# Kernel tuning notes

Measured on AMD Instinct MI355X. Metric: run time of the kernel, lower is better.

Reference implementation:

```python
import jax, jax.numpy as jnp
import numpy as np

NEG_SLOPE = 0.1
K = 3  # kernel_size

def lrelu(x):
    return jnp.where(x >= 0, x, NEG_SLOPE * x)

def setup_inputs() -> dict:
    key = jax.random.key(0)
    ks = jax.random.split(key, 10)
    B, C, H, W = 16, 64, 128, 128
    DEG, RED = 512, 8
    s = 0.02
    return {
        "feat": jax.random.normal(ks[0], (B, C, H, W), jnp.float32),
        "deg": jax.random.normal(ks[1], (B, DEG, 8, 8), jnp.float32),
        # adaptive_size: Linear(deg_fsize -> C), no bias; torch weight [out,in]
        "W_size": jax.random.normal(ks[2], (C, DEG), jnp.float32) * s,
        # kernel net: Linear(C -> C//red), Linear(C//red -> C*K*K)
        "W_k1": jax.random.normal(ks[3], (C // RED, C), jnp.float32) * s,
        "W_k2": jax.random.normal(ks[4], (C * K * K, C // RED), jnp.float32) * s,
        # 1x1 conv C_in -> C_out with bias (stored as [out,in])
        "W_conv": jax.random.normal(ks[5], (C, C), jnp.float32) * s,
        "b_conv": jax.random.normal(ks[6], (C,), jnp.float32) * s,
        # CA layer: 1x1 conv deg_fsize -> C, then C -> C//red -> C
        "W_ac": jax.random.normal(ks[7], (C, DEG), jnp.float32) * s,
        "W_du1": jax.random.normal(ks[8], (C // RED, C), jnp.float32) * s,
        "W_du2": jax.random.normal(ks[9], (C, C // RED), jnp.float32) * s,
    }

def reference(feat, deg, W_size, W_k1, W_k2, W_conv, b_conv, W_ac, W_du1, W_du2):
    b, c, h, w = feat.shape
    # degradation pooled to a vector: AdaptiveAvgPool2d((1,1)) == mean over HW
    dvec = deg.mean(axis=(2, 3))                      # [B, deg_fsize]
    f = dvec @ W_size.T                               # [B, C]
    # per-sample dynamic depthwise kernels
    kern = lrelu(f @ W_k1.T) @ W_k2.T                 # [B, C*K*K]
    kern = kern.reshape(b * c, 1, K, K)               # [B*C, 1, K, K]
    out = jax.lax.conv_general_dilated(
        feat.reshape(1, b * c, h, w), kern,
        window_strides=(1, 1), padding=[((K - 1) // 2,) * 2] * 2,
        feature_group_count=b * c,
        dimension_numbers=("NCHW", "OIHW", "NCHW"))
    out = lrelu(out).reshape(b, c, h, w)
    # trailing 1x1 conv with bias
    out = jnp.einsum("bchw,oc->bohw", out, W_conv) + b_conv[None, :, None, None]
    # CA branch
    fa = dvec @ W_ac.T                                # [B, C]
    att = jax.nn.sigmoid(lrelu(fa @ W_du1.T) @ W_du2.T)  # [B, C_out]
    return out + feat * att[:, :, None, None]
```

## Files before the change

kernel.cpp:

```cpp
#include <hip/hip_runtime.h>
#include <math.h>

#define NEG_SLOPE 0.1f

typedef __attribute__((ext_vector_type(8))) short short8;
typedef __attribute__((ext_vector_type(4))) short short4v;
typedef __attribute__((ext_vector_type(4))) float floatx4;

__device__ __forceinline__ float lrelu(float x) { return x >= 0.0f ? x : NEG_SLOPE * x; }

__device__ __forceinline__ unsigned short f2bf(float x) {
  unsigned u = __float_as_uint(x);
  return (unsigned short)((u + 0x7fffu + ((u >> 16) & 1u)) >> 16);
}

__device__ __forceinline__ float wave_sum64(float v) {
  #pragma unroll
  for (int s = 32; s > 0; s >>= 1) v += __shfl_xor(v, s, 64);
  return v;
}

__global__ __launch_bounds__(256) void prep_kernel(
    const float* __restrict__ deg, const float* __restrict__ W_size,
    const float* __restrict__ W_k1, const float* __restrict__ W_k2,
    const float* __restrict__ W_ac, const float* __restrict__ W_du1,
    const float* __restrict__ W_du2, float* __restrict__ kern_ws,
    float* __restrict__ att_ws) {
  const int b = blockIdx.x;
  const int t = threadIdx.x;
  __shared__ float dvec[512];
  __shared__ float fbuf[64], fabuf[64];
  __shared__ float t1s[8], t2s[8];

  const float* degb = deg + (size_t)b * 32768;
  const int half = t & 1, row0 = t >> 1;
  #pragma unroll
  for (int u = 0; u < 4; ++u) {
    const int d = row0 + u * 128;
    const float* p = degb + (size_t)d * 64 + half * 32;
    float4 x0 = *(const float4*)(p);
    float4 x1 = *(const float4*)(p + 4);
    float4 x2 = *(const float4*)(p + 8);
    float4 x3 = *(const float4*)(p + 12);
    float4 x4 = *(const float4*)(p + 16);
    float4 x5 = *(const float4*)(p + 20);
    float4 x6 = *(const float4*)(p + 24);
    float4 x7 = *(const float4*)(p + 28);
    float s = (x0.x + x0.y + x0.z + x0.w) + (x1.x + x1.y + x1.z + x1.w) +
              (x2.x + x2.y + x2.z + x2.w) + (x3.x + x3.y + x3.z + x3.w) +
              (x4.x + x4.y + x4.z + x4.w) + (x5.x + x5.y + x5.z + x5.w) +
              (x6.x + x6.y + x6.z + x6.w) + (x7.x + x7.y + x7.z + x7.w);
    s += __shfl_xor(s, 1, 64);
    if (half == 0) dvec[d] = s * (1.0f / 64.0f);
  }
  __syncthreads();

  {
    const int c = t >> 2, q = t & 3;
    const float* w1 = W_size + (size_t)c * 512;
    const float* w2 = W_ac + (size_t)c * 512;
    float p1 = 0.0f, p2 = 0.0f;
    #pragma unroll 4
    for (int kk = 0; kk < 32; ++kk) {
      const int e = kk * 16 + q * 4;
      float4 d4 = *(const float4*)&dvec[e];
      float4 a4 = *(const float4*)(w1 + e);
      float4 b4 = *(const float4*)(w2 + e);
      p1 += d4.x * a4.x + d4.y * a4.y + d4.z * a4.z + d4.w * a4.w;
      p2 += d4.x * b4.x + d4.y * b4.y + d4.z * b4.z + d4.w * b4.w;
    }
    p1 += __shfl_xor(p1, 1, 64); p1 += __shfl_xor(p1, 2, 64);
    p2 += __shfl_xor(p2, 1, 64); p2 += __shfl_xor(p2, 2, 64);
    if (q == 0) { fbuf[c] = p1; fabuf[c] = p2; }
  }
  __syncthreads();

  const int wave = t >> 6, lane = t & 63;
  if (wave == 0) {
    float v = fbuf[lane];
    #pragma unroll
    for (int rr = 0; rr < 8; ++rr) {
      float p = wave_sum64(v * W_k1[rr * 64 + lane]);
      if (lane == 0) t1s[rr] = lrelu(p);
    }
  } else if (wave == 1) {
    float v = fabuf[lane];
    #pragma unroll
    for (int rr = 0; rr < 8; ++rr) {
      float p = wave_sum64(v * W_du1[rr * 64 + lane]);
      if (lane == 0) t2s[rr] = lrelu(p);
    }
  }
  __syncthreads();

  for (int i = t; i < 576; i += 256) {
    float4 wa0 = *(const float4*)&W_k2[i * 8];
    float4 wa1 = *(const float4*)&W_k2[i * 8 + 4];
    kern_ws[b * 576 + i] =
        t1s[0] * wa0.x + t1s[1] * wa0.y + t1s[2] * wa0.z + t1s[3] * wa0.w +
        t1s[4] * wa1.x + t1s[5] * wa1.y + t1s[6] * wa1.z + t1s[7] * wa1.w;
  }
  if (t < 64) {
    float4 wa0 = *(const float4*)&W_du2[t * 8];
    float4 wa1 = *(const float4*)&W_du2[t * 8 + 4];
    float s = t2s[0] * wa0.x + t2s[1] * wa0.y + t2s[2] * wa0.z + t2s[3] * wa0.w +
              t2s[4] * wa1.x + t2s[5] * wa1.y + t2s[6] * wa1.z + t2s[7] * wa1.w;
    att_ws[b * 64 + t] = 1.0f / (1.0f + expf(-s));
  }
}

__global__ __launch_bounds__(256, 5) void fused_kernel(
    const float* __restrict__ feat, const float* __restrict__ W_conv,
    const float* __restrict__ b_conv, const float* __restrict__ kern_ws,
    const float* __restrict__ att_ws, float* __restrict__ out) {
  const int bid = blockIdx.x;
  const int b = bid >> 7;
  const int h = bid & 127;

  const int t = threadIdx.x;

  __shared__ __align__(16) unsigned short zT[128 * 72];
  __shared__ __align__(16) unsigned short wt[64 * 72];
  __shared__ float ks[576];
  __shared__ float atts[64];
  __shared__ float bcs[64];

  {
    const int o = t >> 2;
    const int c0 = (t & 3) * 16;
    const float* wp = W_conv + o * 64 + c0;
    float4 a0 = *(const float4*)(wp);
    float4 a1 = *(const float4*)(wp + 4);
    float4 a2 = *(const float4*)(wp + 8);
    float4 a3 = *(const float4*)(wp + 12);
    const int sw = ((o >> 2) ^ (o >> 5)) & 7;
    short8 p0, p1;
    p0[0] = f2bf(a0.x); p0[1] = f2bf(a0.y); p0[2] = f2bf(a0.z); p0[3] = f2bf(a0.w);
    p0[4] = f2bf(a1.x); p0[5] = f2bf(a1.y); p0[6] = f2bf(a1.z); p0[7] = f2bf(a1.w);
    p1[0] = f2bf(a2.x); p1[1] = f2bf(a2.y); p1[2] = f2bf(a2.z); p1[3] = f2bf(a2.w);
    p1[4] = f2bf(a3.x); p1[5] = f2bf(a3.y); p1[6] = f2bf(a3.z); p1[7] = f2bf(a3.w);
    const int kc0 = ((c0 >> 3) + 0) ^ sw;
    const int kc1 = ((c0 >> 3) + 1) ^ sw;
    *(short8*)&wt[o * 72 + kc0 * 8] = p0;
    *(short8*)&wt[o * 72 + kc1 * 8] = p1;
  }
  for (int i = t; i < 576; i += 256) ks[i] = kern_ws[b * 576 + i];
  if (t < 64) { atts[t] = att_ws[b * 64 + t]; bcs[t] = b_conv[t]; }
  __syncthreads();

  const size_t base_b = (size_t)b * 64 * 128 * 128;
  const int lane = t & 63, wave = t >> 6;
  const int cq = t >> 5;
  const int gg = t & 31;
  const int w0 = gg * 4;
  const int swz = (gg ^ (gg >> 3)) & 7;
  const float4 zf4 = {0.f, 0.f, 0.f, 0.f};

  const bool hgt0 = (h > 0), hlt = (h < 127);
  const float* fbase = feat + base_b + (size_t)h * 128 + w0;

  #pragma unroll
  for (int it = 0; it < 2; ++it) {
    const int c0 = cq * 4 + it * 32;
    float4 top[4], mid[4], bot[4];
    #pragma unroll
    for (int j = 0; j < 4; ++j) {
      const float* p = fbase + (size_t)(c0 + j) * 16384;
      mid[j] = *(const float4*)p;
      top[j] = hgt0 ? *(const float4*)(p - 128) : zf4;
      bot[j] = hlt  ? *(const float4*)(p + 128) : zf4;
    }
    unsigned short sres[4][4];
    #pragma unroll
    for (int j = 0; j < 4; ++j) {
      const float* kv = &ks[(c0 + j) * 9];
      const float k0 = kv[0], k1 = kv[1], k2 = kv[2];
      const float k3 = kv[3], k4 = kv[4], k5 = kv[5];
      const float k6 = kv[6], k7 = kv[7], k8 = kv[8];
      float a0 = 0.f, a1 = 0.f, a2 = 0.f, a3 = 0.f;
      {
        float4 m = top[j];
        float lf = __shfl(m.w, lane - 1, 64); if (gg == 0)  lf = 0.f;
        float rt = __shfl(m.x, lane + 1, 64); if (gg == 31) rt = 0.f;
        a0 += k0 * lf  + k1 * m.x + k2 * m.y;
        a1 += k0 * m.x + k1 * m.y + k2 * m.z;
        a2 += k0 * m.y + k1 * m.z + k2 * m.w;
        a3 += k0 * m.z + k1 * m.w + k2 * rt;
      }
      {
        float4 m = mid[j];
        float lf = __shfl(m.w, lane - 1, 64); if (gg == 0)  lf = 0.f;
        float rt = __shfl(m.x, lane + 1, 64); if (gg == 31) rt = 0.f;
        a0 += k3 * lf  + k4 * m.x + k5 * m.y;
        a1 += k3 * m.x + k4 * m.y + k5 * m.z;
        a2 += k3 * m.y + k4 * m.z + k5 * m.w;
        a3 += k3 * m.z + k4 * m.w + k5 * rt;
      }
      {
        float4 m = bot[j];
        float lf = __shfl(m.w, lane - 1, 64); if (gg == 0)  lf = 0.f;
        float rt = __shfl(m.x, lane + 1, 64); if (gg == 31) rt = 0.f;
        a0 += k6 * lf  + k7 * m.x + k8 * m.y;
        a1 += k6 * m.x + k7 * m.y + k8 * m.z;
        a2 += k6 * m.y + k7 * m.z + k8 * m.w;
        a3 += k6 * m.z + k7 * m.w + k8 * rt;
      }
      sres[j][0] = f2bf(lrelu(a0));
      sres[j][1] = f2bf(lrelu(a1));
      sres[j][2] = f2bf(lrelu(a2));
      sres[j][3] = f2bf(lrelu(a3));
    }
    const int chunk = (cq >> 1) + it * 4;
    const int kcs = ((chunk ^ swz) * 8) + (cq & 1) * 4;
    #pragma unroll
    for (int i = 0; i < 4; ++i) {
      short4v sv;
      sv[0] = (short)sres[0][i]; sv[1] = (short)sres[1][i];
      sv[2] = (short)sres[2][i]; sv[3] = (short)sres[3][i];
      *(short4v*)&zT[(w0 + i) * 72 + kcs] = sv;
    }
  }
  __syncthreads();

  {
    const int r = lane & 15, q = lane >> 4;

    short8 az[2][2];
    #pragma unroll
    for (int wm2 = 0; wm2 < 2; ++wm2) {
      const int w = (wave * 2 + wm2) * 16 + r;
      const int sz = ((w >> 2) ^ (w >> 5)) & 7;
      #pragma unroll
      for (int ksp = 0; ksp < 2; ++ksp) {
        const int kc = (ksp * 4 + q) ^ sz;
        az[wm2][ksp] = *(const short8*)&zT[w * 72 + kc * 8];
      }
    }
    short8 bw[4][2];
    #pragma unroll
    for (int nt = 0; nt < 4; ++nt) {
      const int o = nt * 16 + r;
      const int so = ((o >> 2) ^ (o >> 5)) & 7;
      #pragma unroll
      for (int ksp = 0; ksp < 2; ++ksp) {
        const int kc = (ksp * 4 + q) ^ so;
        bw[nt][ksp] = *(const short8*)&wt[o * 72 + kc * 8];
      }
    }

    floatx4 acc[2][4];
    #pragma unroll
    for (int wm2 = 0; wm2 < 2; ++wm2)
      #pragma unroll
      for (int nt = 0; nt < 4; ++nt) acc[wm2][nt] = (floatx4){0.f, 0.f, 0.f, 0.f};

    #pragma unroll
    for (int wm2 = 0; wm2 < 2; ++wm2)
      #pragma unroll
      for (int nt = 0; nt < 4; ++nt)
        #pragma unroll
        for (int ksp = 0; ksp < 2; ++ksp)
          acc[wm2][nt] = __builtin_amdgcn_mfma_f32_16x16x32_bf16(
              az[wm2][ksp], bw[nt][ksp], acc[wm2][nt], 0, 0, 0);

    #pragma unroll
    for (int wm2 = 0; wm2 < 2; ++wm2) {
      const int wb = (wave * 2 + wm2) * 16 + q * 4;
      #pragma unroll
      for (int nt = 0; nt < 4; ++nt) {
        const int o = nt * 16 + r;
        const size_t off = base_b + (size_t)o * 16384 + (size_t)h * 128 + wb;
        float4 fv = *(const float4*)(feat + off);
        const float at = atts[o], bo = bcs[o];
        floatx4 a = acc[wm2][nt];
        float4 ov;
        ov.x = a[0] + bo + at * fv.x;
        ov.y = a[1] + bo + at * fv.y;
        ov.z = a[2] + bo + at * fv.z;
        ov.w = a[3] + bo + at * fv.w;
        *(float4*)(out + off) = ov;
      }
    }
  }
}

extern "C" void kernel_launch(void* const* d_in, const int* in_sizes, int n_in,
                              void* d_out, int out_size, void* d_ws, size_t ws_size,
                              hipStream_t stream) {
  const float* feat   = (const float*)d_in[0];
  const float* deg    = (const float*)d_in[1];
  const float* W_size = (const float*)d_in[2];
  const float* W_k1   = (const float*)d_in[3];
  const float* W_k2   = (const float*)d_in[4];
  const float* W_conv = (const float*)d_in[5];
  const float* b_conv = (const float*)d_in[6];
  const float* W_ac   = (const float*)d_in[7];
  const float* W_du1  = (const float*)d_in[8];
  const float* W_du2  = (const float*)d_in[9];
  float* out = (float*)d_out;

  float* kern_ws = (float*)d_ws;
  float* att_ws  = kern_ws + 16 * 576;

  prep_kernel<<<16, 256, 0, stream>>>(deg, W_size, W_k1, W_k2, W_ac, W_du1,
                                      W_du2, kern_ws, att_ws);
  fused_kernel<<<2048, 256, 0, stream>>>(feat, W_conv, b_conv, kern_ws, att_ws,
                                         out);
}
```

Before: 180.0 us.

## Process two rows per workgroup to reuse halo loads and weight setup

Each workgroup now computes two output rows, loading four input rows instead of three per output row. This cuts the vertical halo reloads and amortises the per-block W_conv bf16 conversion and kernel/attention staging over twice the work. Block IDs are remapped across XCDs, and the launch bound drops to 4 waves per SIMD to make room for the extra registers. The costs are fewer blocks (1024), higher register pressure, and extra LDS syncs between the two MFMA epilogues.

```diff
diff --git a/kernel.cpp b/kernel.cpp
--- a/kernel.cpp
+++ b/kernel.cpp
@@ -109,13 +109,69 @@
   }
 }
 
-__global__ __launch_bounds__(256, 5) void fused_kernel(
+__device__ __forceinline__ void load_az(const unsigned short* zT, int lane,
+                                        int wave, short8 az[2][2]) {
+  const int r = lane & 15, q = lane >> 4;
+  #pragma unroll
+  for (int wm2 = 0; wm2 < 2; ++wm2) {
+    const int w = (wave * 2 + wm2) * 16 + r;
+    const int sz = ((w >> 2) ^ (w >> 5)) & 7;
+    #pragma unroll
+    for (int ksp = 0; ksp < 2; ++ksp) {
+      const int kc = (ksp * 4 + q) ^ sz;
+      az[wm2][ksp] = *(const short8*)&zT[w * 72 + kc * 8];
+    }
+  }
+}
+
+__device__ __forceinline__ void mfma_epilogue(
+    const short8 az[2][2], const short8 bw[4][2], const float* atts,
+    const float* bcs, const float* __restrict__ feat, float* __restrict__ out,
+    size_t base_b, int h, int lane, int wave) {
+  const int r = lane & 15, q = lane >> 4;
+  floatx4 acc[2][4];
+  #pragma unroll
+  for (int wm2 = 0; wm2 < 2; ++wm2)
+    #pragma unroll
+    for (int nt = 0; nt < 4; ++nt) acc[wm2][nt] = (floatx4){0.f, 0.f, 0.f, 0.f};
+
+  #pragma unroll
+  for (int wm2 = 0; wm2 < 2; ++wm2)
+    #pragma unroll
+    for (int nt = 0; nt < 4; ++nt)
+      #pragma unroll
+      for (int ksp = 0; ksp < 2; ++ksp)
+        acc[wm2][nt] = __builtin_amdgcn_mfma_f32_16x16x32_bf16(
+            az[wm2][ksp], bw[nt][ksp], acc[wm2][nt], 0, 0, 0);
+
+  #pragma unroll
+  for (int wm2 = 0; wm2 < 2; ++wm2) {
+    const int wb = (wave * 2 + wm2) * 16 + q * 4;
+    #pragma unroll
+    for (int nt = 0; nt < 4; ++nt) {
+      const int o = nt * 16 + r;
+      const size_t off = base_b + (size_t)o * 16384 + (size_t)h * 128 + wb;
+      float4 fv = *(const float4*)(feat + off);
+      const float at = atts[o], bo = bcs[o];
+      floatx4 a = acc[wm2][nt];
+      float4 ov;
+      ov.x = a[0] + bo + at * fv.x;
+      ov.y = a[1] + bo + at * fv.y;
+      ov.z = a[2] + bo + at * fv.z;
+      ov.w = a[3] + bo + at * fv.w;
+      *(float4*)(out + off) = ov;
+    }
+  }
+}
+
+__global__ __launch_bounds__(256, 4) void fused_kernel(
     const float* __restrict__ feat, const float* __restrict__ W_conv,
     const float* __restrict__ b_conv, const float* __restrict__ kern_ws,
     const float* __restrict__ att_ws, float* __restrict__ out) {
-  const int bid = blockIdx.x;
-  const int b = bid >> 7;
-  const int h = bid & 127;
+  const int raw = blockIdx.x;
+  const int wg = (raw & 7) * 128 + (raw >> 3);
+  const int b = wg >> 6;
+  const int h0 = (wg & 63) << 1;
 
   const int t = threadIdx.x;
 
@@ -156,87 +212,100 @@
   const int swz = (gg ^ (gg >> 3)) & 7;
   const float4 zf4 = {0.f, 0.f, 0.f, 0.f};
 
-  const bool hgt0 = (h > 0), hlt = (h < 127);
-  const float* fbase = feat + base_b + (size_t)h * 128 + w0;
+  const bool has_r0 = (h0 > 0);
+  const bool has_r3 = (h0 < 126);
+  const float* fbase = feat + base_b + (size_t)h0 * 128 + w0;
+
+  short4v sv1[2][4];
 
   #pragma unroll
   for (int it = 0; it < 2; ++it) {
     const int c0 = cq * 4 + it * 32;
-    float4 top[4], mid[4], bot[4];
+    float4 r0[4], r1[4], r2[4], r3[4];
     #pragma unroll
     for (int j = 0; j < 4; ++j) {
       const float* p = fbase + (size_t)(c0 + j) * 16384;
-      mid[j] = *(const float4*)p;
-      top[j] = hgt0 ? *(const float4*)(p - 128) : zf4;
-      bot[j] = hlt  ? *(const float4*)(p + 128) : zf4;
-    }
-    unsigned short sres[4][4];
+      r1[j] = *(const float4*)p;
+      r2[j] = *(const float4*)(p + 128);
+      r0[j] = has_r0 ? *(const float4*)(p - 128) : zf4;
+      r3[j] = has_r3 ? *(const float4*)(p + 256) : zf4;
+    }
+    unsigned short s0[4][4], s1[4][4];
     #pragma unroll
     for (int j = 0; j < 4; ++j) {
       const float* kv = &ks[(c0 + j) * 9];
       const float k0 = kv[0], k1 = kv[1], k2 = kv[2];
       const float k3 = kv[3], k4 = kv[4], k5 = kv[5];
       const float k6 = kv[6], k7 = kv[7], k8 = kv[8];
+      float lf0 = __shfl(r0[j].w, lane - 1, 64), rt0 = __shfl(r0[j].x, lane + 1, 64);
+      float lf1 = __shfl(r1[j].w, lane - 1, 64), rt1 = __shfl(r1[j].x, lane + 1, 64);
+      float lf2 = __shfl(r2[j].w, lane - 1, 64), rt2 = __shfl(r2[j].x, lane + 1, 64);
+      float lf3 = __shfl(r3[j].w, lane - 1, 64), rt3 = __shfl(r3[j].x, lane + 1, 64);
+      if (gg == 0)  { lf0 = lf1 = lf2 = lf3 = 0.f; }
+      if (gg == 31) { rt0 = rt1 = rt2 = rt3 = 0.f; }
+
       float a0 = 0.f, a1 = 0.f, a2 = 0.f, a3 = 0.f;
+      float b0 = 0.f, b1 = 0.f, b2 = 0.f, b3 = 0.f;
       {
-        float4 m = top[j];
-        float lf = __shfl(m.w, lane - 1, 64); if (gg == 0)  lf = 0.f;
-        float rt = __shfl(m.x, lane + 1, 64); if (gg == 31) rt = 0.f;
-        a0 += k0 * lf  + k1 * m.x + k2 * m.y;
+        float4 m = r0[j];
+        a0 += k0 * lf0 + k1 * m.x + k2 * m.y;
         a1 += k0 * m.x + k1 * m.y + k2 * m.z;
         a2 += k0 * m.y + k1 * m.z + k2 * m.w;
-        a3 += k0 * m.z + k1 * m.w + k2 * rt;
+        a3 += k0 * m.z + k1 * m.w + k2 * rt0;
       }
       {
-        float4 m = mid[j];
-        float lf = __shfl(m.w, lane - 1, 64); if (gg == 0)  lf = 0.f;
-        float rt = __shfl(m.x, lane + 1, 64); if (gg == 31) rt = 0.f;
-        a0 += k3 * lf  + k4 * m.x + k5 * m.y;
+        float4 m = r1[j];
+        a0 += k3 * lf1 + k4 * m.x + k5 * m.y;
         a1 += k3 * m.x + k4 * m.y + k5 * m.z;
         a2 += k3 * m.y + k4 * m.z + k5 * m.w;
-        a3 += k3 * m.z + k4 * m.w + k5 * rt;
+        a3 += k3 * m.z + k4 * m.w + k5 * rt1;
+        b0 += k0 * lf1 + k1 * m.x + k2 * m.y;
+        b1 += k0 * m.x + k1 * m.y + k2 * m.z;
+        b2 += k0 * m.y + k1 * m.z + k2 * m.w;
+        b3 += k0 * m.z + k1 * m.w + k2 * rt1;
       }
       {
-        float4 m = bot[j];
-        float lf = __shfl(m.w, lane - 1, 64); if (gg == 0)  lf = 0.f;
-        float rt = __shfl(m.x, lane + 1, 64); if (gg == 31) rt = 0.f;
-        a0 += k6 * lf  + k7 * m.x + k8 * m.y;
+        float4 m = r2[j];
+        a0 += k6 * lf2 + k7 * m.x + k8 * m.y;
         a1 += k6 * m.x + k7 * m.y + k8 * m.z;
         a2 += k6 * m.y + k7 * m.z + k8 * m.w;
-        a3 += k6 * m.z + k7 * m.w + k8 * rt;
-      }
-      sres[j][0] = f2bf(lrelu(a0));
-      sres[j][1] = f2bf(lrelu(a1));
-      sres[j][2] = f2bf(lrelu(a2));
-      sres[j][3] = f2bf(lrelu(a3));
+        a3 += k6 * m.z + k7 * m.w + k8 * rt2;
+        b0 += k3 * lf2 + k4 * m.x + k5 * m.y;
+        b1 += k3 * m.x + k4 * m.y + k5 * m.z;
+        b2 += k3 * m.y + k4 * m.z + k5 * m.w;
+        b3 += k3 * m.z + k4 * m.w + k5 * rt2;
+      }
+      {
+        float4 m = r3[j];
+        b0 += k6 * lf3 + k7 * m.x + k8 * m.y;
+        b1 += k6 * m.x + k7 * m.y + k8 * m.z;
+        b2 += k6 * m.y + k7 * m.z + k8 * m.w;
+        b3 += k6 * m.z + k7 * m.w + k8 * rt3;
+      }
+      s0[j][0] = f2bf(lrelu(a0)); s0[j][1] = f2bf(lrelu(a1));
+      s0[j][2] = f2bf(lrelu(a2)); s0[j][3] = f2bf(lrelu(a3));
+      s1[j][0] = f2bf(lrelu(b0)); s1[j][1] = f2bf(lrelu(b1));
+      s1[j][2] = f2bf(lrelu(b2)); s1[j][3] = f2bf(lrelu(b3));
     }
     const int chunk = (cq >> 1) + it * 4;
     const int kcs = ((chunk ^ swz) * 8) + (cq & 1) * 4;
     #pragma unroll
     for (int i = 0; i < 4; ++i) {
       short4v sv;
-      sv[0] = (short)sres[0][i]; sv[1] = (short)sres[1][i];
-      sv[2] = (short)sres[2][i]; sv[3] = (short)sres[3][i];
+      sv[0] = (short)s0[0][i]; sv[1] = (short)s0[1][i];
+      sv[2] = (short)s0[2][i]; sv[3] = (short)s0[3][i];
       *(short4v*)&zT[(w0 + i) * 72 + kcs] = sv;
-    }
-  }
-  __syncthreads();
-
+      short4v tv;
+      tv[0] = (short)s1[0][i]; tv[1] = (short)s1[1][i];
+      tv[2] = (short)s1[2][i]; tv[3] = (short)s1[3][i];
+      sv1[it][i] = tv;
+    }
+  }
+  __syncthreads();
+
+  short8 bw[4][2];
   {
     const int r = lane & 15, q = lane >> 4;
-
-    short8 az[2][2];
-    #pragma unroll
-    for (int wm2 = 0; wm2 < 2; ++wm2) {
-      const int w = (wave * 2 + wm2) * 16 + r;
-      const int sz = ((w >> 2) ^ (w >> 5)) & 7;
-      #pragma unroll
-      for (int ksp = 0; ksp < 2; ++ksp) {
-        const int kc = (ksp * 4 + q) ^ sz;
-        az[wm2][ksp] = *(const short8*)&zT[w * 72 + kc * 8];
-      }
-    }
-    short8 bw[4][2];
     #pragma unroll
     for (int nt = 0; nt < 4; ++nt) {
       const int o = nt * 16 + r;
@@ -247,41 +316,25 @@
         bw[nt][ksp] = *(const short8*)&wt[o * 72 + kc * 8];
       }
     }
-
-    floatx4 acc[2][4];
-    #pragma unroll
-    for (int wm2 = 0; wm2 < 2; ++wm2)
-      #pragma unroll
-      for (int nt = 0; nt < 4; ++nt) acc[wm2][nt] = (floatx4){0.f, 0.f, 0.f, 0.f};
-
-    #pragma unroll
-    for (int wm2 = 0; wm2 < 2; ++wm2)
-      #pragma unroll
-      for (int nt = 0; nt < 4; ++nt)
-        #pragma unroll
-        for (int ksp = 0; ksp < 2; ++ksp)
-          acc[wm2][nt] = __builtin_amdgcn_mfma_f32_16x16x32_bf16(
-              az[wm2][ksp], bw[nt][ksp], acc[wm2][nt], 0, 0, 0);
-
-    #pragma unroll
-    for (int wm2 = 0; wm2 < 2; ++wm2) {
-      const int wb = (wave * 2 + wm2) * 16 + q * 4;
-      #pragma unroll
-      for (int nt = 0; nt < 4; ++nt) {
-        const int o = nt * 16 + r;
-        const size_t off = base_b + (size_t)o * 16384 + (size_t)h * 128 + wb;
-        float4 fv = *(const float4*)(feat + off);
-        const float at = atts[o], bo = bcs[o];
-        floatx4 a = acc[wm2][nt];
-        float4 ov;
-        ov.x = a[0] + bo + at * fv.x;
-        ov.y = a[1] + bo + at * fv.y;
-        ov.z = a[2] + bo + at * fv.z;
-        ov.w = a[3] + bo + at * fv.w;
-        *(float4*)(out + off) = ov;
-      }
-    }
-  }
+  }
+  short8 az[2][2];
+  load_az(zT, lane, wave, az);
+  __syncthreads();
+
+  #pragma unroll
+  for (int it = 0; it < 2; ++it) {
+    const int chunk = (cq >> 1) + it * 4;
+    const int kcs = ((chunk ^ swz) * 8) + (cq & 1) * 4;
+    #pragma unroll
+    for (int i = 0; i < 4; ++i)
+      *(short4v*)&zT[(w0 + i) * 72 + kcs] = sv1[it][i];
+  }
+
+  mfma_epilogue(az, bw, atts, bcs, feat, out, base_b, h0, lane, wave);
+  __syncthreads();
+
+  load_az(zT, lane, wave, az);
+  mfma_epilogue(az, bw, atts, bcs, feat, out, base_b, h0 + 1, lane, wave);
 }
 
 extern "C" void kernel_launch(void* const* d_in, const int* in_sizes, int n_in,
@@ -304,6 +357,6 @@
 
   prep_kernel<<<16, 256, 0, stream>>>(deg, W_size, W_k1, W_k2, W_ac, W_du1,
                                       W_du2, kern_ws, att_ws);
-  fused_kernel<<<2048, 256, 0, stream>>>(feat, W_conv, b_conv, kern_ws, att_ws,
+  fused_kernel<<<1024, 256, 0, stream>>>(feat, W_conv, b_conv, kern_ws, att_ws,
                                          out);
 }
```

Result: slower. 234.3 us (+30.2%).

## Split prep kernel into three launches to spread pooling and matvec across more blocks

Applied to the files above, without the earlier changes.

The single 16-block prep kernel is replaced by three kernels: deg pooling over 64 blocks, the two 512-wide matvecs over 128 blocks, and the small kernel/attention tail over 16 blocks. Intermediate vectors now go through workspace in global memory. The aim is to use more CUs for the serial prep phase, which only had 16 blocks. The cost is two extra kernel launches and global round-trips.

```diff
diff --git a/kernel.cpp b/kernel.cpp
--- a/kernel.cpp
+++ b/kernel.cpp
@@ -20,71 +20,78 @@
   return v;
 }
 
-__global__ __launch_bounds__(256) void prep_kernel(
-    const float* __restrict__ deg, const float* __restrict__ W_size,
+__global__ __launch_bounds__(256) void prep_dvec(
+    const float* __restrict__ deg, float* __restrict__ dvec_ws) {
+  const int b = blockIdx.x >> 2;
+  const int quarter = blockIdx.x & 3;
+  const int t = threadIdx.x;
+  const int half = t & 1, row = t >> 1;
+  const int d = quarter * 128 + row;
+  const float* p = deg + (size_t)b * 32768 + (size_t)d * 64 + half * 32;
+  float4 x0 = *(const float4*)(p);
+  float4 x1 = *(const float4*)(p + 4);
+  float4 x2 = *(const float4*)(p + 8);
+  float4 x3 = *(const float4*)(p + 12);
+  float4 x4 = *(const float4*)(p + 16);
+  float4 x5 = *(const float4*)(p + 20);
+  float4 x6 = *(const float4*)(p + 24);
+  float4 x7 = *(const float4*)(p + 28);
+  float s = (x0.x + x0.y + x0.z + x0.w) + (x1.x + x1.y + x1.z + x1.w) +
+            (x2.x + x2.y + x2.z + x2.w) + (x3.x + x3.y + x3.z + x3.w) +
+            (x4.x + x4.y + x4.z + x4.w) + (x5.x + x5.y + x5.z + x5.w) +
+            (x6.x + x6.y + x6.z + x6.w) + (x7.x + x7.y + x7.z + x7.w);
+  s += __shfl_xor(s, 1, 64);
+  if (half == 0) dvec_ws[b * 512 + d] = s * (1.0f / 64.0f);
+}
+
+__global__ __launch_bounds__(256) void prep_fmul(
+    const float* __restrict__ W_size, const float* __restrict__ W_ac,
+    const float* __restrict__ dvec_ws, float* __restrict__ f_ws,
+    float* __restrict__ fa_ws) {
+  const int b = blockIdx.x >> 3;
+  const int g = blockIdx.x & 7;
+  const int t = threadIdx.x;
+  const int dot = t >> 4;
+  const int s = t & 15;
+  const int c = g * 8 + (dot & 7);
+  const float* wr =
+      (dot < 8 ? W_size + (size_t)c * 512 : W_ac + (size_t)c * 512) + s * 32;
+  const float* dv = dvec_ws + b * 512 + s * 32;
+  float p = 0.0f;
+  #pragma unroll
+  for (int k = 0; k < 8; ++k) {
+    float4 w4 = *(const float4*)(wr + k * 4);
+    float4 d4 = *(const float4*)(dv + k * 4);
+    p += w4.x * d4.x + w4.y * d4.y + w4.z * d4.z + w4.w * d4.w;
+  }
+  p += __shfl_xor(p, 1, 64);
+  p += __shfl_xor(p, 2, 64);
+  p += __shfl_xor(p, 4, 64);
+  p += __shfl_xor(p, 8, 64);
+  if (s == 0) {
+    if (dot < 8) f_ws[b * 64 + c] = p;
+    else         fa_ws[b * 64 + c] = p;
+  }
+}
+
+__global__ __launch_bounds__(256) void prep_tail(
     const float* __restrict__ W_k1, const float* __restrict__ W_k2,
-    const float* __restrict__ W_ac, const float* __restrict__ W_du1,
-    const float* __restrict__ W_du2, float* __restrict__ kern_ws,
-    float* __restrict__ att_ws) {
+    const float* __restrict__ W_du1, const float* __restrict__ W_du2,
+    const float* __restrict__ f_ws, const float* __restrict__ fa_ws,
+    float* __restrict__ kern_ws, float* __restrict__ att_ws) {
   const int b = blockIdx.x;
   const int t = threadIdx.x;
-  __shared__ float dvec[512];
-  __shared__ float fbuf[64], fabuf[64];
   __shared__ float t1s[8], t2s[8];
-
-  const float* degb = deg + (size_t)b * 32768;
-  const int half = t & 1, row0 = t >> 1;
-  #pragma unroll
-  for (int u = 0; u < 4; ++u) {
-    const int d = row0 + u * 128;
-    const float* p = degb + (size_t)d * 64 + half * 32;
-    float4 x0 = *(const float4*)(p);
-    float4 x1 = *(const float4*)(p + 4);
-    float4 x2 = *(const float4*)(p + 8);
-    float4 x3 = *(const float4*)(p + 12);
-    float4 x4 = *(const float4*)(p + 16);
-    float4 x5 = *(const float4*)(p + 20);
-    float4 x6 = *(const float4*)(p + 24);
-    float4 x7 = *(const float4*)(p + 28);
-    float s = (x0.x + x0.y + x0.z + x0.w) + (x1.x + x1.y + x1.z + x1.w) +
-              (x2.x + x2.y + x2.z + x2.w) + (x3.x + x3.y + x3.z + x3.w) +
-              (x4.x + x4.y + x4.z + x4.w) + (x5.x + x5.y + x5.z + x5.w) +
-              (x6.x + x6.y + x6.z + x6.w) + (x7.x + x7.y + x7.z + x7.w);
-    s += __shfl_xor(s, 1, 64);
-    if (half == 0) dvec[d] = s * (1.0f / 64.0f);
-  }
-  __syncthreads();
-
-  {
-    const int c = t >> 2, q = t & 3;
-    const float* w1 = W_size + (size_t)c * 512;
-    const float* w2 = W_ac + (size_t)c * 512;
-    float p1 = 0.0f, p2 = 0.0f;
-    #pragma unroll 4
-    for (int kk = 0; kk < 32; ++kk) {
-      const int e = kk * 16 + q * 4;
-      float4 d4 = *(const float4*)&dvec[e];
-      float4 a4 = *(const float4*)(w1 + e);
-      float4 b4 = *(const float4*)(w2 + e);
-      p1 += d4.x * a4.x + d4.y * a4.y + d4.z * a4.z + d4.w * a4.w;
-      p2 += d4.x * b4.x + d4.y * b4.y + d4.z * b4.z + d4.w * b4.w;
-    }
-    p1 += __shfl_xor(p1, 1, 64); p1 += __shfl_xor(p1, 2, 64);
-    p2 += __shfl_xor(p2, 1, 64); p2 += __shfl_xor(p2, 2, 64);
-    if (q == 0) { fbuf[c] = p1; fabuf[c] = p2; }
-  }
-  __syncthreads();
-
   const int wave = t >> 6, lane = t & 63;
   if (wave == 0) {
-    float v = fbuf[lane];
+    float v = f_ws[b * 64 + lane];
     #pragma unroll
     for (int rr = 0; rr < 8; ++rr) {
       float p = wave_sum64(v * W_k1[rr * 64 + lane]);
       if (lane == 0) t1s[rr] = lrelu(p);
     }
   } else if (wave == 1) {
-    float v = fabuf[lane];
+    float v = fa_ws[b * 64 + lane];
     #pragma unroll
     for (int rr = 0; rr < 8; ++rr) {
       float p = wave_sum64(v * W_du1[rr * 64 + lane]);
@@ -301,9 +308,14 @@
 
   float* kern_ws = (float*)d_ws;
   float* att_ws  = kern_ws + 16 * 576;
-
-  prep_kernel<<<16, 256, 0, stream>>>(deg, W_size, W_k1, W_k2, W_ac, W_du1,
-                                      W_du2, kern_ws, att_ws);
+  float* dvec_ws = att_ws + 16 * 64;
+  float* f_ws    = dvec_ws + 16 * 512;
+  float* fa_ws   = f_ws + 16 * 64;
+
+  prep_dvec<<<64, 256, 0, stream>>>(deg, dvec_ws);
+  prep_fmul<<<128, 256, 0, stream>>>(W_size, W_ac, dvec_ws, f_ws, fa_ws);
+  prep_tail<<<16, 256, 0, stream>>>(W_k1, W_k2, W_du1, W_du2, f_ws, fa_ws,
+                                    kern_ws, att_ws);
   fused_kernel<<<2048, 256, 0, stream>>>(feat, W_conv, b_conv, kern_ws, att_ws,
                                          out);
 }
```

Measured after the change: 175.8 us. 1.02x faster.
